# Optimization experiments

Hardware: AMD Instinct MI355X
Metric: run time of the kernel (lower is better)

The kernel has to match this reference:

```python
import jax, jax.numpy as jnp
import numpy as np
import math

N_EMBD = 512
N_HEAD = 8
B, T = 2, 4096


def setup_inputs() -> dict:
    key = jax.random.key(0)
    ks = jax.random.split(key, 12)
    s = 1.0 / math.sqrt(N_EMBD)
    inp = {
        "x": jax.random.normal(ks[0], (B, T, N_EMBD), dtype=jnp.float32),
        "weight": jax.random.uniform(ks[1], (1,), dtype=jnp.float32),
        "state": jax.random.uniform(ks[2], (1,), dtype=jnp.float32),
        "Wq": jax.random.normal(ks[3], (N_EMBD, N_EMBD), dtype=jnp.float32) * s,
        "bq": jnp.zeros((N_EMBD,), dtype=jnp.float32),
        "Wk": jax.random.normal(ks[4], (N_EMBD, N_EMBD), dtype=jnp.float32) * s,
        "bk": jnp.zeros((N_EMBD,), dtype=jnp.float32),
        "Wv": jax.random.normal(ks[5], (N_EMBD, N_EMBD), dtype=jnp.float32) * s,
        "bv": jnp.zeros((N_EMBD,), dtype=jnp.float32),
        "Wp": jax.random.normal(ks[6], (N_EMBD, N_EMBD), dtype=jnp.float32) * s,
        "bp": jnp.zeros((N_EMBD,), dtype=jnp.float32),
    }
    return inp


def reference(x, weight, state, Wq, bq, Wk, bk, Wv, bv, Wp, bp):
    # weight / state are accepted but unused, matching the torch module.
    Bb, Tt, C = x.shape
    hd = C // N_HEAD

    def split_heads(t):  # [B,T,C] -> [B,H,T,hd]
        return t.reshape(Bb, Tt, N_HEAD, hd).transpose(0, 2, 1, 3)

    # torch nn.Linear: y = x @ W.T + b
    q = split_heads(x @ Wq.T + bq)
    k = split_heads(x @ Wk.T + bk)
    v = split_heads(x @ Wv.T + bv)

    scale = 1.0 / math.sqrt(hd)
    att = jnp.einsum("bhqd,bhkd->bhqk", q, k) * scale  # [B,H,T,T]
    causal = jnp.tril(jnp.ones((Tt, Tt), dtype=bool))
    att = jnp.where(causal[None, None, :, :], att, -jnp.inf)
    att = jax.nn.softmax(att, axis=-1)
    # attn_drop / resid_drop are identity (p=0 / eval)
    y = jnp.einsum("bhqk,bhkd->bhqd", att, v)  # [B,H,T,hd]
    y = y.transpose(0, 2, 1, 3).reshape(Bb, Tt, C)
    return y @ Wp.T + bp
```

## Files before the change

### kernel.cpp

```cpp
#include <hip/hip_runtime.h>
#include <math.h>

using short8  = __attribute__((ext_vector_type(8))) short;
using floatx4 = __attribute__((ext_vector_type(4))) float;

#define DEVI __device__ __forceinline__

#define BATCH 2
#define SEQ   4096
#define NE    512
#define NH    8
#define HD    64
#define MTOT  8192

#define QSCALE 0.18033688011112042f

DEVI short f2bf(float f) {
    unsigned u = __builtin_bit_cast(unsigned, f);
    unsigned r = (u + 0x7fffu + ((u >> 16) & 1u)) >> 16;
    return (short)r;
}

DEVI void async16(const void* g, void* l) {
    __builtin_amdgcn_global_load_lds(
        (const __attribute__((address_space(1))) void*)g,
        (__attribute__((address_space(3))) void*)l, 16, 0, 0);
}

__global__ __launch_bounds__(256) void cvt_all(const float* __restrict__ x,
                                               const float* __restrict__ wq,
                                               const float* __restrict__ wk,
                                               const float* __restrict__ wv,
                                               const float* __restrict__ wp,
                                               short* __restrict__ xbf,
                                               short* __restrict__ wbf) {
    int i = blockIdx.x * 256 + threadIdx.x;
    const float* src; short* dst; int off;
    if (i < MTOT * NE / 4) {
        src = x; dst = xbf; off = i;
    } else {
        int j = i - MTOT * NE / 4;
        int wsel = j >> 16;
        off = j & 65535;
        src = (wsel == 0) ? wq : (wsel == 1) ? wk : (wsel == 2) ? wv : wp;
        dst = wbf + (size_t)wsel * NE * NE;
    }
    float4 f = ((const float4*)src)[off];
    short4 o;
    o.x = f2bf(f.x); o.y = f2bf(f.y); o.z = f2bf(f.z); o.w = f2bf(f.w);
    ((short4*)dst)[off] = o;
}

DEVI void gemm_mainloop(const short* __restrict__ A, const short* __restrict__ W,
                        int m0, int n0, short* ldsA, short* ldsW, floatx4 (&acc)[4][4]) {
    const int tid  = threadIdx.x;
    const int lane = tid & 63;
    const int w    = tid >> 6;
    const int wm   = w >> 1, wn = w & 1;
    const int quad = lane >> 4, l15 = lane & 15;
    const int srow = lane >> 3, scol = (lane & 7) * 8;

    for (int i = 0; i < 4; ++i)
        for (int j = 0; j < 4; ++j)
            acc[i][j] = floatx4{0.f, 0.f, 0.f, 0.f};

    for (int kt = 0; kt < NE / 64; ++kt) {
        const int k0 = kt * 64;
        for (int c = 0; c < 4; ++c) {
            const int rb = w * 32 + c * 8;
            async16(A + (size_t)(m0 + rb + srow) * NE + k0 + scol, ldsA + rb * 64);
            async16(W + (size_t)(n0 + rb + srow) * NE + k0 + scol, ldsW + rb * 64);
        }
        __syncthreads();
        for (int ks = 0; ks < 2; ++ks) {
            short8 af[4], bf[4];
            for (int i = 0; i < 4; ++i)
                af[i] = *(const short8*)(ldsA + (wm * 64 + i * 16 + l15) * 64 + ks * 32 + quad * 8);
            for (int j = 0; j < 4; ++j)
                bf[j] = *(const short8*)(ldsW + (wn * 64 + j * 16 + l15) * 64 + ks * 32 + quad * 8);
            for (int i = 0; i < 4; ++i)
                for (int j = 0; j < 4; ++j)
                    acc[i][j] = __builtin_amdgcn_mfma_f32_16x16x32_bf16(af[i], bf[j], acc[i][j], 0, 0, 0);
        }
        __syncthreads();
    }
}

__global__ __launch_bounds__(256) void gemm_qkv(const short* __restrict__ xbf,
                                                const short* __restrict__ wbf,
                                                const float* __restrict__ bq,
                                                const float* __restrict__ bk,
                                                const float* __restrict__ bv,
                                                short* __restrict__ qkv) {
    __shared__ short lds[128 * 132];
    short* ldsA = lds;
    short* ldsW = lds + 128 * 64;
    const int m0 = blockIdx.x * 128, n0 = blockIdx.y * 128, z = blockIdx.z;
    const short* W = wbf + (size_t)z * (NE * NE);
    short* out = qkv + (size_t)z * (MTOT * NE);

    floatx4 acc[4][4];
    gemm_mainloop(xbf, W, m0, n0, ldsA, ldsW, acc);

    const int tid = threadIdx.x;
    const int lane = tid & 63, w = tid >> 6;
    const int wm = w >> 1, wn = w & 1, quad = lane >> 4, l15 = lane & 15;
    const int b = m0 >> 12, t0 = m0 & 4095;

    if (z == 2) {
        for (int j = 0; j < 4; ++j) {
            const int dl = wn * 64 + j * 16 + l15;
            const float bz = bv[n0 + dl];
            for (int i = 0; i < 4; ++i) {
                const int tl0 = wm * 64 + i * 16 + quad * 4;
                short4 o;
                o.x = f2bf(acc[i][j][0] + bz);
                o.y = f2bf(acc[i][j][1] + bz);
                o.z = f2bf(acc[i][j][2] + bz);
                o.w = f2bf(acc[i][j][3] + bz);
                *(short4*)&lds[dl * 132 + tl0] = o;
            }
        }
        __syncthreads();
        const int tc = tid & 15, dr = tid >> 4;
        for (int p = 0; p < 8; ++p) {
            const int dl = p * 16 + dr;
            const int colg = n0 + dl;
            const int hg = colg >> 6, d = colg & 63;
            short8 v = *(short8*)&lds[dl * 132 + tc * 8];
            *(short8*)&out[((size_t)(b * NH + hg) * HD + d) * SEQ + t0 + tc * 8] = v;
        }
    } else {
        const float* bias = (z == 0) ? bq : bk;
        const float scale = (z == 0) ? QSCALE : 1.0f;
        for (int j = 0; j < 4; ++j) {
            const int dl = wn * 64 + j * 16 + l15;
            const float bz = bias[n0 + dl];
            for (int i = 0; i < 4; ++i) {
                for (int r = 0; r < 4; ++r) {
                    const int tl = wm * 64 + i * 16 + quad * 4 + r;
                    lds[tl * 132 + dl] = f2bf((acc[i][j][r] + bz) * scale);
                }
            }
        }
        __syncthreads();
        const int hsel = tid >> 7;
        const int dc = tid & 7, trow = (tid >> 3) & 15;
        const int hg = (n0 + hsel * 64) >> 6;
        short* outbase = out + ((size_t)(b * NH + hg) * SEQ + t0) * HD;
        for (int p = 0; p < 8; ++p) {
            const int tl = p * 16 + trow;
            short8 v = *(short8*)&lds[tl * 132 + hsel * 64 + dc * 8];
            *(short8*)&outbase[(size_t)tl * HD + dc * 8] = v;
        }
    }
}

__global__ __launch_bounds__(256) void gemm_proj(const short* __restrict__ ybf,
                                                 const short* __restrict__ wp,
                                                 const float* __restrict__ bp,
                                                 float* __restrict__ out) {
    __shared__ short ldsA[128 * 64];
    __shared__ short ldsW[128 * 64];
    const int m0 = blockIdx.x * 128, n0 = blockIdx.y * 128;

    floatx4 acc[4][4];
    gemm_mainloop(ybf, wp, m0, n0, ldsA, ldsW, acc);

    const int lane = threadIdx.x & 63, w = threadIdx.x >> 6;
    const int wm = w >> 1, wn = w & 1, quad = lane >> 4, l15 = lane & 15;
    for (int j = 0; j < 4; ++j) {
        const int col = n0 + wn * 64 + j * 16 + l15;
        const float bz = bp[col];
        for (int i = 0; i < 4; ++i) {
            for (int r = 0; r < 4; ++r) {
                const int row = m0 + wm * 64 + i * 16 + quad * 4 + r;
                out[(size_t)row * NE + col] = acc[i][j][r] + bz;
            }
        }
    }
}

template<bool DOMASK>
DEVI void attn_subtile(const short* __restrict__ bK, const short* __restrict__ bV,
                       const short8 (&qfrag)[2], short* __restrict__ myP,
                       floatx4 (&O)[4], float (&lsum)[4],
                       const int p0, const int p1, const int quad, const int l15,
                       const int w) {
    short8 kf[2][4], vf[2][4];
#pragma unroll
    for (int n = 0; n < 4; ++n) {
        const int row = n * 16 + l15;
        kf[0][n] = *(const short8*)(bK + row * 64 + p0 * 8);
        kf[1][n] = *(const short8*)(bK + row * 64 + p1 * 8);
        vf[0][n] = *(const short8*)(bV + row * 64 + p0 * 8);
        vf[1][n] = *(const short8*)(bV + row * 64 + p1 * 8);
    }

    floatx4 S[4];
#pragma unroll
    for (int n = 0; n < 4; ++n) S[n] = floatx4{0.f, 0.f, 0.f, 0.f};
    __builtin_amdgcn_s_setprio(1);
#pragma unroll
    for (int ks = 0; ks < 2; ++ks)
#pragma unroll
        for (int n = 0; n < 4; ++n)
            S[n] = __builtin_amdgcn_mfma_f32_16x16x32_bf16(qfrag[ks], kf[ks][n], S[n], 0, 0, 0);
    __builtin_amdgcn_s_setprio(0);

    if (DOMASK) {
#pragma unroll
        for (int n = 0; n < 4; ++n)
#pragma unroll
            for (int r = 0; r < 4; ++r) {
                const int rowl = w * 16 + quad * 4 + r;
                const int coll = n * 16 + l15;
                if (coll > rowl) S[n][r] = -3.0e38f;
            }
    }

#pragma unroll
    for (int n = 0; n < 4; ++n)
#pragma unroll
        for (int r = 0; r < 4; ++r)
            S[n][r] = __builtin_amdgcn_exp2f(S[n][r]);
#pragma unroll
    for (int r = 0; r < 4; ++r)
        lsum[r] += (S[0][r] + S[1][r]) + (S[2][r] + S[3][r]);

#pragma unroll
    for (int n = 0; n < 4; ++n)
#pragma unroll
        for (int r = 0; r < 4; ++r)
            myP[(quad * 4 + r) * 72 + n * 16 + l15] = f2bf(S[n][r]);

    short8 pf[2];
#pragma unroll
    for (int ks = 0; ks < 2; ++ks)
        pf[ks] = *(const short8*)(myP + l15 * 72 + ks * 32 + quad * 8);

    __builtin_amdgcn_s_setprio(1);
#pragma unroll
    for (int ks = 0; ks < 2; ++ks)
#pragma unroll
        for (int n = 0; n < 4; ++n)
            O[n] = __builtin_amdgcn_mfma_f32_16x16x32_bf16(pf[ks], vf[ks][n], O[n], 0, 0, 0);
    __builtin_amdgcn_s_setprio(0);
}

__global__ __launch_bounds__(256, 2) void attn(const short* __restrict__ q,
                                               const short* __restrict__ k,
                                               const short* __restrict__ vt,
                                               short* __restrict__ y) {
    const int id = blockIdx.x;
    const int bx = id >> 4;
    const int bh = ((id & 7) << 1) | ((id >> 3) & 1);
    const int tid = threadIdx.x, lane = tid & 63, w = tid >> 6;
    const int quad = lane >> 4, l15 = lane & 15;

    __shared__ short ldsK[2][2][64 * 64];
    __shared__ short ldsV[2][2][64 * 64];
    __shared__ short ldsP[4][16 * 72];

    const short* K  = k  + (size_t)bh * (SEQ * HD);
    const short* VT = vt + (size_t)bh * (HD * SEQ);
    short* myP = (short*)ldsP[w];
    const int b = bh >> 3, h = bh & 7;

    const int lb   = ((lane & 7) - (lane >> 3)) & 7;
    const int jrow = lane >> 3;
    const int p0 = (quad + (l15 & 7)) & 7;
    const int p1 = p0 ^ 4;

    for (int sel = 0; sel < 2; ++sel) {
        const int qt = sel ? (SEQ / 64 - 1 - bx) : bx;
        const short* Q = q + (size_t)bh * (SEQ * HD) + (size_t)qt * 64 * HD;

        short8 qfrag[2];
#pragma unroll
        for (int ks = 0; ks < 2; ++ks)
            qfrag[ks] = *(const short8*)&Q[(w * 16 + l15) * HD + ks * 32 + quad * 8];

        floatx4 O[4];
        float lsum[4];
#pragma unroll
        for (int n = 0; n < 4; ++n) O[n] = floatx4{0.f, 0.f, 0.f, 0.f};
#pragma unroll
        for (int r = 0; r < 4; ++r) lsum[r] = 0.f;

        const int npair = (qt >> 1) + 1;

        __syncthreads();
#pragma unroll
        for (int s = 0; s < 2; ++s) {
            const short* Kt = K + (size_t)s * 64 * HD;
            const short* Vc = VT + s * 64;
#pragma unroll
            for (int c2 = 0; c2 < 2; ++c2) {
                const int chunk = w * 2 + c2;
                const int j = chunk * 8 + jrow;
                async16(Kt + (size_t)j * HD + lb * 8, ldsK[0][s] + chunk * 512);
                async16(Vc + (size_t)j * SEQ + lb * 8, ldsV[0][s] + chunk * 512);
            }
        }

        for (int p = 0; p + 1 < npair; ++p) {
            __syncthreads();
            const int pipe = p & 1, nx = pipe ^ 1;

#pragma unroll
            for (int s = 0; s < 2; ++s) {
                const int js = 2 * (p + 1) + s;
                const short* Kt = K + (size_t)js * 64 * HD;
                const short* Vc = VT + js * 64;
#pragma unroll
                for (int c2 = 0; c2 < 2; ++c2) {
                    const int chunk = w * 2 + c2;
                    const int j = chunk * 8 + jrow;
                    async16(Kt + (size_t)j * HD + lb * 8, ldsK[nx][s] + chunk * 512);
                    async16(Vc + (size_t)j * SEQ + lb * 8, ldsV[nx][s] + chunk * 512);
                }
            }

            attn_subtile<false>(ldsK[pipe][0], ldsV[pipe][0], qfrag, myP, O, lsum,
                                p0, p1, quad, l15, w);
            attn_subtile<false>(ldsK[pipe][1], ldsV[pipe][1], qfrag, myP, O, lsum,
                                p0, p1, quad, l15, w);
        }

        {
            __syncthreads();
            const int ep = (npair - 1) & 1;
            if (qt & 1) {
                attn_subtile<false>(ldsK[ep][0], ldsV[ep][0], qfrag, myP, O, lsum,
                                    p0, p1, quad, l15, w);
                attn_subtile<true >(ldsK[ep][1], ldsV[ep][1], qfrag, myP, O, lsum,
                                    p0, p1, quad, l15, w);
            } else {
                attn_subtile<true >(ldsK[ep][0], ldsV[ep][0], qfrag, myP, O, lsum,
                                    p0, p1, quad, l15, w);
            }
        }

#pragma unroll
        for (int r = 0; r < 4; ++r) {
#pragma unroll
            for (int off = 1; off < 16; off <<= 1)
                lsum[r] += __shfl_xor(lsum[r], off, 64);
        }

#pragma unroll
        for (int r = 0; r < 4; ++r) {
            const float inv = 1.0f / lsum[r];
            const int t = qt * 64 + w * 16 + quad * 4 + r;
#pragma unroll
            for (int n = 0; n < 4; ++n) {
                const int col = h * 64 + n * 16 + l15;
                y[((size_t)(b * SEQ + t)) * NE + col] = f2bf(O[n][r] * inv);
            }
        }
    }
}

extern "C" void kernel_launch(void* const* d_in, const int* in_sizes, int n_in,
                              void* d_out, int out_size, void* d_ws, size_t ws_size,
                              hipStream_t stream) {
    const float* x  = (const float*)d_in[0];
    const float* Wq = (const float*)d_in[3];
    const float* bq = (const float*)d_in[4];
    const float* Wk = (const float*)d_in[5];
    const float* bk = (const float*)d_in[6];
    const float* Wv = (const float*)d_in[7];
    const float* bv = (const float*)d_in[8];
    const float* Wp = (const float*)d_in[9];
    const float* bp = (const float*)d_in[10];
    float* out = (float*)d_out;

    short* ws   = (short*)d_ws;
    short* xbf  = ws;
    short* wbf  = xbf + (size_t)MTOT * NE;
    short* qb   = wbf + 4 * (size_t)NE * NE;
    short* kb   = qb + (size_t)MTOT * NE;
    short* vtb  = kb + (size_t)MTOT * NE;
    short* yb   = xbf;

    cvt_all<<<dim3((MTOT * NE / 4 + 4 * NE * NE / 4) / 256), 256, 0, stream>>>(
        x, Wq, Wk, Wv, Wp, xbf, wbf);

    gemm_qkv<<<dim3(MTOT / 128, NE / 128, 3), 256, 0, stream>>>(xbf, wbf, bq, bk, bv, qb);

    attn<<<dim3(512), 256, 0, stream>>>(qb, kb, vtb, yb);

    gemm_proj<<<dim3(MTOT / 128, NE / 128), 256, 0, stream>>>(yb, wbf + 3 * (size_t)NE * NE, bp, out);
}
```

Baseline: 196.9 us.

## Stage one KV tile per step to raise occupancy to three blocks per CU

The attention kernel's K/V staging is reduced from two 64-key sub-tiles per pipeline step to a single 64-key tile, with a double buffer per tile. This halves the LDS footprint, and launch bounds are raised so three blocks can be resident per compute unit instead of two. The aim is more latency hiding through occupancy. In exchange there are twice as many barriers and prefetch issues per key range, and tighter register limits that may cause spills.

```diff
diff --git a/kernel.cpp b/kernel.cpp
--- a/kernel.cpp
+++ b/kernel.cpp
@@ -248,7 +248,7 @@
     __builtin_amdgcn_s_setprio(0);
 }
 
-__global__ __launch_bounds__(256, 2) void attn(const short* __restrict__ q,
+__global__ __launch_bounds__(256, 3) void attn(const short* __restrict__ q,
                                                const short* __restrict__ k,
                                                const short* __restrict__ vt,
                                                short* __restrict__ y) {
@@ -258,8 +258,8 @@
     const int tid = threadIdx.x, lane = tid & 63, w = tid >> 6;
     const int quad = lane >> 4, l15 = lane & 15;
 
-    __shared__ short ldsK[2][2][64 * 64];
-    __shared__ short ldsV[2][2][64 * 64];
+    __shared__ short ldsK[2][64 * 64];
+    __shared__ short ldsV[2][64 * 64];
     __shared__ short ldsP[4][16 * 72];
 
     const short* K  = k  + (size_t)bh * (SEQ * HD);
@@ -288,59 +288,42 @@
 #pragma unroll
         for (int r = 0; r < 4; ++r) lsum[r] = 0.f;
 
-        const int npair = (qt >> 1) + 1;
-
-        __syncthreads();
-#pragma unroll
-        for (int s = 0; s < 2; ++s) {
-            const short* Kt = K + (size_t)s * 64 * HD;
-            const short* Vc = VT + s * 64;
+        __syncthreads();
+        {
+            const short* Kt = K;
+            const short* Vc = VT;
 #pragma unroll
             for (int c2 = 0; c2 < 2; ++c2) {
                 const int chunk = w * 2 + c2;
                 const int j = chunk * 8 + jrow;
-                async16(Kt + (size_t)j * HD + lb * 8, ldsK[0][s] + chunk * 512);
-                async16(Vc + (size_t)j * SEQ + lb * 8, ldsV[0][s] + chunk * 512);
-            }
-        }
-
-        for (int p = 0; p + 1 < npair; ++p) {
+                async16(Kt + (size_t)j * HD + lb * 8, ldsK[0] + chunk * 512);
+                async16(Vc + (size_t)j * SEQ + lb * 8, ldsV[0] + chunk * 512);
+            }
+        }
+
+        for (int jt = 0; jt < qt; ++jt) {
             __syncthreads();
-            const int pipe = p & 1, nx = pipe ^ 1;
-
-#pragma unroll
-            for (int s = 0; s < 2; ++s) {
-                const int js = 2 * (p + 1) + s;
-                const short* Kt = K + (size_t)js * 64 * HD;
-                const short* Vc = VT + js * 64;
+            const int cur = jt & 1, nxt = cur ^ 1;
+
+            {
+                const short* Kt = K + (size_t)(jt + 1) * 64 * HD;
+                const short* Vc = VT + (jt + 1) * 64;
 #pragma unroll
                 for (int c2 = 0; c2 < 2; ++c2) {
                     const int chunk = w * 2 + c2;
                     const int j = chunk * 8 + jrow;
-                    async16(Kt + (size_t)j * HD + lb * 8, ldsK[nx][s] + chunk * 512);
-                    async16(Vc + (size_t)j * SEQ + lb * 8, ldsV[nx][s] + chunk * 512);
+                    async16(Kt + (size_t)j * HD + lb * 8, ldsK[nxt] + chunk * 512);
+                    async16(Vc + (size_t)j * SEQ + lb * 8, ldsV[nxt] + chunk * 512);
                 }
             }
 
-            attn_subtile<false>(ldsK[pipe][0], ldsV[pipe][0], qfrag, myP, O, lsum,
+            attn_subtile<false>(ldsK[cur], ldsV[cur], qfrag, myP, O, lsum,
                                 p0, p1, quad, l15, w);
-            attn_subtile<false>(ldsK[pipe][1], ldsV[pipe][1], qfrag, myP, O, lsum,
-                                p0, p1, quad, l15, w);
-        }
-
-        {
-            __syncthreads();
-            const int ep = (npair - 1) & 1;
-            if (qt & 1) {
-                attn_subtile<false>(ldsK[ep][0], ldsV[ep][0], qfrag, myP, O, lsum,
-                                    p0, p1, quad, l15, w);
-                attn_subtile<true >(ldsK[ep][1], ldsV[ep][1], qfrag, myP, O, lsum,
-                                    p0, p1, quad, l15, w);
-            } else {
-                attn_subtile<true >(ldsK[ep][0], ldsV[ep][0], qfrag, myP, O, lsum,
-                                    p0, p1, quad, l15, w);
-            }
-        }
+        }
+
+        __syncthreads();
+        attn_subtile<true>(ldsK[qt & 1], ldsV[qt & 1], qfrag, myP, O, lsum,
+                           p0, p1, quad, l15, w);
 
 #pragma unroll
         for (int r = 0; r < 4; ++r) {
```

Result: no change. 198.9 us (+1.0%).
